# Kernel optimization log

Hardware: AMD Instinct MI355X
Metric: run time of the kernel (lower is better)

## Reference

```python
import jax, jax.numpy as jnp
import numpy as np

N_HEADS = 16
HEAD_DIM = 64
D_MODEL = N_HEADS * HEAD_DIM
MASK_NUM = -2.0**32 + 1.0
LN_EPS = 1e-8


def setup_inputs() -> dict:
    key = jax.random.key(0)
    ks = jax.random.split(key, 6)
    B, S = 2, 2048
    queries = jax.random.normal(ks[0], (B, S, D_MODEL), dtype=jnp.float32)
    keys = jax.random.normal(ks[1], (B, S, D_MODEL), dtype=jnp.float32)
    values = jax.random.normal(ks[2], (B, S, D_MODEL), dtype=jnp.float32)
    lim = np.sqrt(6.0 / (D_MODEL + D_MODEL)).astype(np.float32)  # glorot_uniform
    Wq = jax.random.uniform(ks[3], (D_MODEL, D_MODEL), jnp.float32, -lim, lim)
    Wk = jax.random.uniform(ks[4], (D_MODEL, D_MODEL), jnp.float32, -lim, lim)
    Wv = jax.random.uniform(ks[5], (D_MODEL, D_MODEL), jnp.float32, -lim, lim)
    gamma = jnp.ones((D_MODEL,), jnp.float32)
    beta = jnp.zeros((D_MODEL,), jnp.float32)
    return {"queries": queries, "keys": keys, "values": values,
            "Wq": Wq, "Wk": Wk, "Wv": Wv, "gamma": gamma, "beta": beta}


def _split_heads(x):
    # [B, S, H*dh] -> tf.split(axis=2)+concat(axis=0) order: [H*B, S, dh]
    B, S, _ = x.shape
    return x.reshape(B, S, N_HEADS, HEAD_DIM).transpose(2, 0, 1, 3).reshape(N_HEADS * B, S, HEAD_DIM)


def _merge_heads(x, B):
    # [H*B, S, dh] -> [B, S, H*dh]
    S = x.shape[1]
    return x.reshape(N_HEADS, B, S, HEAD_DIM).transpose(1, 2, 0, 3).reshape(B, S, D_MODEL)


def reference(queries, keys, values, Wq, Wk, Wv, gamma, beta):
    B = queries.shape[0]
    q = _split_heads(queries @ Wq)   # [HB, Sq, dh]
    k = _split_heads(keys @ Wk)      # [HB, Sk, dh]
    v = _split_heads(values @ Wv)    # [HB, Sk, dh]

    scores = jnp.einsum('bqd,bkd->bqk', q, k) / jnp.float32(np.sqrt(HEAD_DIM))
    # key padding mask: positions whose projected key is all-zero
    kmask = jnp.sign(jnp.sum(jnp.abs(k), axis=-1))  # [HB, Sk]
    scores = jnp.where(kmask[:, None, :] == 0, jnp.float32(MASK_NUM), scores)
    attn = jax.nn.softmax(scores, axis=-1)
    # query mask: zero out rows whose projected query is all-zero
    qmask = jnp.sign(jnp.sum(jnp.abs(q), axis=-1))  # [HB, Sq]
    attn = attn * qmask[:, :, None]
    att_out = jnp.einsum('bqk,bkd->bqd', attn, v)   # [HB, Sq, dh]
    att_out = _merge_heads(att_out, B)               # [B, Sq, D]

    x = att_out + queries
    mean = jnp.mean(x, axis=-1, keepdims=True)
    var = jnp.mean((x - mean) ** 2, axis=-1, keepdims=True)
    norm = (x - mean) / jnp.sqrt(var + LN_EPS)
    return gamma * norm + beta
```

## Files before the change

### kernel.cpp

```cpp
#include <hip/hip_runtime.h>

#define DM   1024
#define SEQ  2048
#define NH   16
#define HD   64
#define ROWS 4096

typedef unsigned short u16;
typedef unsigned int   u32;
typedef __attribute__((ext_vector_type(8))) __bf16 bf16x8;
typedef __attribute__((ext_vector_type(4))) float  f32x4;
typedef __attribute__((ext_vector_type(16))) float f32x16;

__device__ __forceinline__ u16 f2bf(float f) {
  u32 u = __builtin_bit_cast(u32, f);
  u += 0x7fffu + ((u >> 16) & 1u);
  return (u16)(u >> 16);
}

__device__ __forceinline__ void async16(const void* g, void* lds) {
  __builtin_amdgcn_global_load_lds((const __attribute__((address_space(1))) u32*)g,
                                   (__attribute__((address_space(3))) u32*)lds, 16, 0, 0);
}


__global__ __launch_bounds__(256) void k_cvt_act(const float* __restrict__ q,
                                                 const float* __restrict__ k,
                                                 const float* __restrict__ v,
                                                 u16* __restrict__ dst) {
  const float* src = blockIdx.z == 0 ? q : (blockIdx.z == 1 ? k : v);
  u16* d = dst + (size_t)blockIdx.z * ((size_t)ROWS * DM);
  size_t i = ((size_t)blockIdx.x * 256 + threadIdx.x) * 8;
  float4 a = *(const float4*)(src + i);
  float4 b = *(const float4*)(src + i + 4);
  u32 w0 = (u32)f2bf(a.x) | ((u32)f2bf(a.y) << 16);
  u32 w1 = (u32)f2bf(a.z) | ((u32)f2bf(a.w) << 16);
  u32 w2 = (u32)f2bf(b.x) | ((u32)f2bf(b.y) << 16);
  u32 w3 = (u32)f2bf(b.z) | ((u32)f2bf(b.w) << 16);
  uint4 o4; o4.x = w0; o4.y = w1; o4.z = w2; o4.w = w3;
  *(uint4*)(d + i) = o4;
}

__global__ __launch_bounds__(256) void k_cvt_wt(const float* __restrict__ Wq,
                                                const float* __restrict__ Wk,
                                                const float* __restrict__ Wv,
                                                u16* __restrict__ wt) {
  __shared__ float t[32][33];
  const float* W = blockIdx.z == 0 ? Wq : (blockIdx.z == 1 ? Wk : Wv);
  u16* D = wt + (size_t)blockIdx.z * (DM * DM);
  int bx = blockIdx.x * 32, by = blockIdx.y * 32;
  int x = threadIdx.x, y = threadIdx.y;
  for (int i = 0; i < 32; i += 8) t[y + i][x] = W[(size_t)(by + y + i) * DM + bx + x];
  __syncthreads();
  for (int i = 0; i < 32; i += 8) D[(size_t)(bx + y + i) * DM + by + x] = f2bf(t[x][y + i]);
}


__global__ __launch_bounds__(256) void k_gemm(const u16* __restrict__ Abase,
                                              const u16* __restrict__ Btbase,
                                              u16* __restrict__ Cbase) {
  __shared__ u16 As[128 * 32];
  __shared__ u16 Bs[128 * 32];
  const int z = blockIdx.z;
  const u16* A  = Abase  + (size_t)z * ((size_t)ROWS * DM);
  const u16* Bt = Btbase + (size_t)z * (DM * DM);
  u16* C        = Cbase  + (size_t)z * ((size_t)ROWS * DM);
  const float sc = (z == 0) ? 0.18033688011112043f : 1.0f;
  int tid = threadIdx.x, w = tid >> 6, l = tid & 63;
  int fr = l & 15, fq = l >> 4;
  int bid = blockIdx.y * 8 + blockIdx.x;
  int nb  = (bid & 7) * 32 + (bid >> 3);
  int m0 = (nb >> 3) * 128, n0 = (nb & 7) * 128;
  int wr = (w >> 1) * 64, wc = (w & 1) * 64;
  f32x4 acc[4][4];
  for (int i = 0; i < 4; ++i) for (int j = 0; j < 4; ++j) acc[i][j] = (f32x4){0.f, 0.f, 0.f, 0.f};

  for (int k0 = 0; k0 < DM; k0 += 32) {
    __syncthreads();
    for (int c = 0; c < 2; ++c) {
      int loff = (c * 4 + w) * 1024;
      int eoff = (loff >> 1) + l * 8;
      int row = eoff >> 5;
      int blk = (eoff & 31) >> 3;
      int gblk = blk ^ ((row >> 1) & 3);
      async16(A  + (size_t)(m0 + row) * DM + k0 + (gblk << 3), (char*)As + loff);
      async16(Bt + (size_t)(n0 + row) * DM + k0 + (gblk << 3), (char*)Bs + loff);
    }
    __syncthreads();
    bf16x8 af[4], bf[4];
    for (int i = 0; i < 4; ++i) {
      int row = wr + i * 16 + fr;
      af[i] = *(const bf16x8*)(As + row * 32 + ((fq ^ ((row >> 1) & 3)) << 3));
    }
    for (int j = 0; j < 4; ++j) {
      int row = wc + j * 16 + fr;
      bf[j] = *(const bf16x8*)(Bs + row * 32 + ((fq ^ ((row >> 1) & 3)) << 3));
    }
    for (int i = 0; i < 4; ++i)
      for (int j = 0; j < 4; ++j)
        acc[i][j] = __builtin_amdgcn_mfma_f32_16x16x32_bf16(af[i], bf[j], acc[i][j], 0, 0, 0);
  }
  for (int i = 0; i < 4; ++i)
    for (int j = 0; j < 4; ++j)
      for (int jj = 0; jj < 4; ++jj) {
        int row = m0 + wr + i * 16 + fq * 4 + jj;
        int col = n0 + wc + j * 16 + fr;
        C[(size_t)row * DM + col] = f2bf(acc[i][j][jj] * sc);
      }
}


__global__ __launch_bounds__(256) void k_vt(const u16* __restrict__ vproj,
                                            u16* __restrict__ vt) {
  __shared__ u16 t[64][64];
  int y = blockIdx.y;
  int h = y >> 1, b = y & 1;
  int s0 = blockIdx.x * 64;
  int tid = threadIdx.x;
  for (int c = 0; c < 2; ++c) {
    int rr = c * 32 + (tid >> 3);
    int blk = tid & 7;
    uint4 vv = *(const uint4*)(vproj + (size_t)(b * SEQ + s0 + rr) * DM + h * 64 + blk * 8);
    *(uint4*)(&t[rr][((blk ^ (rr & 7)) * 8)]) = vv;
  }
  __syncthreads();
  for (int c = 0; c < 2; ++c) {
    int d = c * 32 + (tid >> 3);
    int p = tid & 7;
    int B = p ^ (d & 7);
    int g = B >> 1, half = B & 1;
    u16 tmp[8];
    for (int j = 0; j < 8; ++j) {
      int kj = (j < 4) ? (4 * half + j) : (8 + 4 * half + (j - 4));
      int ss = 16 * g + kj;
      tmp[j] = t[ss][((d >> 3) ^ (ss & 7)) * 8 + (d & 7)];
    }
    *(uint4*)(vt + (size_t)(y * 64 + d) * SEQ + s0 + p * 8) = *(uint4*)tmp;
  }
}


__global__ __launch_bounds__(256, 2) void k_attn(const u16* __restrict__ Qp,
                                                 const u16* __restrict__ Kp,
                                                 const u16* __restrict__ Vt,
                                                 float* __restrict__ att) {
  __shared__ u16 lds[20480];
  const int tid = threadIdx.x, w = tid >> 6, l = tid & 63;
  const int lrow = l & 31, h = l >> 5;
  const int kh = w & 1, qg = w >> 1;
  const int g = blockIdx.x;
  const int vy = (g & 7) * 4 + ((g >> 3) & 3);
  const int vx = g >> 5;
  const int head = vy >> 1, b = vy & 1;
  const int hcol = head * 64;
  const int q0w = vx * 128 + qg * 64;

  bf16x8 qb00, qb01, qb02, qb03, qb10, qb11, qb12, qb13;
  {
    const u16* qr0 = Qp + (size_t)(b * SEQ + q0w + lrow) * DM + hcol + h * 8;
    qb00 = *(const bf16x8*)(qr0);
    qb01 = *(const bf16x8*)(qr0 + 16);
    qb02 = *(const bf16x8*)(qr0 + 32);
    qb03 = *(const bf16x8*)(qr0 + 48);
    const u16* qr1 = Qp + (size_t)(b * SEQ + q0w + 32 + lrow) * DM + hcol + h * 8;
    qb10 = *(const bf16x8*)(qr1);
    qb11 = *(const bf16x8*)(qr1 + 16);
    qb12 = *(const bf16x8*)(qr1 + 32);
    qb13 = *(const bf16x8*)(qr1 + 48);
  }

  const int sw = lrow & 7;
  const int kbase = kh * 4096 + lrow * 128;
  const int B0 = kbase + (((0 + h) ^ sw) << 4);
  const int B1 = kbase + (((2 + h) ^ sw) << 4);
  const int B2 = kbase + (((4 + h) ^ sw) << 4);
  const int B3 = kbase + (((6 + h) ^ sw) << 4);

  const int vfb = lrow * 128;
  const int V0 = vfb + (((4 * kh + 0 + h) ^ sw) << 4);
  const int V1 = vfb + (((4 * kh + 2 + h) ^ sw) << 4);

  const int ldo0 = w * 1024, ldo1 = (4 + w) * 1024;
  const int e0 = (ldo0 >> 1) + l * 8, e1 = (ldo1 >> 1) + l * 8;
  const int r0 = e0 >> 6, r1 = e1 >> 6;
  const int kb0 = ((e0 & 63) >> 3) ^ (r0 & 7), kb1 = ((e1 & 63) >> 3) ^ (r1 & 7);
  const u32 koff0 = (u32)((b * SEQ + r0) * DM + hcol + kb0 * 8);
  const u32 koff1 = (u32)((b * SEQ + r1) * DM + hcol + kb1 * 8);
  const u32 voff0 = (u32)((vy * 64 + r0) * SEQ + (e0 & 63));
  const u32 voff1 = (u32)((vy * 64 + r1) * SEQ + (e1 & 63));

  const f32x16 kzero = {};
  f32x16 ot00 = {}, ot01 = {}, ot10 = {}, ot11 = {};
  float lacc0 = 0.f, lacc1 = 0.f;
  bf16x8 pb00 = {}, pb01 = {}, pb10 = {}, pb11 = {};

  char* base = (char*)lds;
  async16(Kp + koff0, base + ldo0);
  async16(Kp + koff1, base + ldo1);
  async16(Vt + voff0, base + 16384 + ldo0);
  async16(Vt + voff1, base + 16384 + ldo1);

  int vwr = 1, vcr = 0, vrd = 2;
  for (int t = 0; t < SEQ / 64; ++t) {
    {
      u32 u = (t + 1 < SEQ / 64) ? (u32)(t + 1) : (u32)(SEQ / 64 - 1);
      u32 kadv = u * (64 * DM);
      u32 vadv = u * 64;
      char* kd = base + ((t + 1) & 1) * 8192;
      char* vd = base + 16384 + vwr * 8192;
      async16(Kp + kadv + koff0, kd + ldo0);
      async16(Kp + kadv + koff1, kd + ldo1);
      async16(Vt + vadv + voff0, vd + ldo0);
      async16(Vt + vadv + voff1, vd + ldo1);
    }
    asm volatile("s_waitcnt vmcnt(6)" ::: "memory");
    __builtin_amdgcn_s_barrier();
    asm volatile("" ::: "memory");

    const char* Kb = base + (t & 1) * 8192;
    bf16x8 a0 = *(const bf16x8*)(Kb + B0);
    bf16x8 a1 = *(const bf16x8*)(Kb + B1);
    bf16x8 a2 = *(const bf16x8*)(Kb + B2);
    bf16x8 a3 = *(const bf16x8*)(Kb + B3);
    __builtin_amdgcn_s_setprio(1);
    f32x16 st0 = __builtin_amdgcn_mfma_f32_32x32x16_bf16(a0, qb00, kzero, 0, 0, 0);
    f32x16 st1 = __builtin_amdgcn_mfma_f32_32x32x16_bf16(a0, qb10, kzero, 0, 0, 0);
    st0 = __builtin_amdgcn_mfma_f32_32x32x16_bf16(a1, qb01, st0, 0, 0, 0);
    st1 = __builtin_amdgcn_mfma_f32_32x32x16_bf16(a1, qb11, st1, 0, 0, 0);
    st0 = __builtin_amdgcn_mfma_f32_32x32x16_bf16(a2, qb02, st0, 0, 0, 0);
    st1 = __builtin_amdgcn_mfma_f32_32x32x16_bf16(a2, qb12, st1, 0, 0, 0);
    st0 = __builtin_amdgcn_mfma_f32_32x32x16_bf16(a3, qb03, st0, 0, 0, 0);
    st1 = __builtin_amdgcn_mfma_f32_32x32x16_bf16(a3, qb13, st1, 0, 0, 0);
    __builtin_amdgcn_s_setprio(0);

    if (t) {
      const char* Vb = base + 16384 + vrd * 8192;
      bf16x8 vf0 = *(const bf16x8*)(Vb + V0);
      bf16x8 vf1 = *(const bf16x8*)(Vb + V1);
      bf16x8 vf2 = *(const bf16x8*)(Vb + 4096 + V0);
      bf16x8 vf3 = *(const bf16x8*)(Vb + 4096 + V1);
      __builtin_amdgcn_s_setprio(1);
      ot00 = __builtin_amdgcn_mfma_f32_32x32x16_bf16(vf0, pb00, ot00, 0, 0, 0);
      ot10 = __builtin_amdgcn_mfma_f32_32x32x16_bf16(vf0, pb10, ot10, 0, 0, 0);
      ot00 = __builtin_amdgcn_mfma_f32_32x32x16_bf16(vf1, pb01, ot00, 0, 0, 0);
      ot10 = __builtin_amdgcn_mfma_f32_32x32x16_bf16(vf1, pb11, ot10, 0, 0, 0);
      ot01 = __builtin_amdgcn_mfma_f32_32x32x16_bf16(vf2, pb00, ot01, 0, 0, 0);
      ot11 = __builtin_amdgcn_mfma_f32_32x32x16_bf16(vf2, pb10, ot11, 0, 0, 0);
      ot01 = __builtin_amdgcn_mfma_f32_32x32x16_bf16(vf3, pb01, ot01, 0, 0, 0);
      ot11 = __builtin_amdgcn_mfma_f32_32x32x16_bf16(vf3, pb11, ot11, 0, 0, 0);
      __builtin_amdgcn_s_setprio(0);
    }

    {
      f32x16 p;
#pragma unroll
      for (int i = 0; i < 16; ++i) p[i] = __builtin_amdgcn_exp2f(st0[i]);
      float s0 = (p[0] + p[1]) + (p[2] + p[3]);
      float s1 = (p[4] + p[5]) + (p[6] + p[7]);
      float s2 = (p[8] + p[9]) + (p[10] + p[11]);
      float s3 = (p[12] + p[13]) + (p[14] + p[15]);
      lacc0 += (s0 + s1) + (s2 + s3);
#pragma unroll
      for (int j = 0; j < 8; ++j) { pb00[j] = (__bf16)p[j]; pb01[j] = (__bf16)p[8 + j]; }
    }
    {
      f32x16 p;
#pragma unroll
      for (int i = 0; i < 16; ++i) p[i] = __builtin_amdgcn_exp2f(st1[i]);
      float s0 = (p[0] + p[1]) + (p[2] + p[3]);
      float s1 = (p[4] + p[5]) + (p[6] + p[7]);
      float s2 = (p[8] + p[9]) + (p[10] + p[11]);
      float s3 = (p[12] + p[13]) + (p[14] + p[15]);
      lacc1 += (s0 + s1) + (s2 + s3);
#pragma unroll
      for (int j = 0; j < 8; ++j) { pb10[j] = (__bf16)p[j]; pb11[j] = (__bf16)p[8 + j]; }
    }

    asm volatile("" ::: "memory");
    __builtin_amdgcn_s_barrier();
    asm volatile("" ::: "memory");

    int tmp = vrd; vrd = vcr; vcr = vwr; vwr = tmp;
  }

  asm volatile("s_waitcnt vmcnt(0)" ::: "memory");
  __builtin_amdgcn_s_barrier();
  asm volatile("" ::: "memory");
  {
    const char* Vb = base + 16384 + vrd * 8192;
    bf16x8 vf0 = *(const bf16x8*)(Vb + V0);
    bf16x8 vf1 = *(const bf16x8*)(Vb + V1);
    bf16x8 vf2 = *(const bf16x8*)(Vb + 4096 + V0);
    bf16x8 vf3 = *(const bf16x8*)(Vb + 4096 + V1);
    ot00 = __builtin_amdgcn_mfma_f32_32x32x16_bf16(vf0, pb00, ot00, 0, 0, 0);
    ot10 = __builtin_amdgcn_mfma_f32_32x32x16_bf16(vf0, pb10, ot10, 0, 0, 0);
    ot00 = __builtin_amdgcn_mfma_f32_32x32x16_bf16(vf1, pb01, ot00, 0, 0, 0);
    ot10 = __builtin_amdgcn_mfma_f32_32x32x16_bf16(vf1, pb11, ot10, 0, 0, 0);
    ot01 = __builtin_amdgcn_mfma_f32_32x32x16_bf16(vf2, pb00, ot01, 0, 0, 0);
    ot11 = __builtin_amdgcn_mfma_f32_32x32x16_bf16(vf2, pb10, ot11, 0, 0, 0);
    ot01 = __builtin_amdgcn_mfma_f32_32x32x16_bf16(vf3, pb01, ot01, 0, 0, 0);
    ot11 = __builtin_amdgcn_mfma_f32_32x32x16_bf16(vf3, pb11, ot11, 0, 0, 0);
  }
  lacc0 += __shfl_xor(lacc0, 32);
  lacc1 += __shfl_xor(lacc1, 32);

  __syncthreads();
  float* mrg = (float*)lds;
  const int slot = qg * 4352;
  if (kh) {
#pragma unroll
    for (int r = 0; r < 16; ++r) {
      mrg[slot + r * 64 + l] = ot00[r];
      mrg[slot + (16 + r) * 64 + l] = ot01[r];
      mrg[slot + (32 + r) * 64 + l] = ot10[r];
      mrg[slot + (48 + r) * 64 + l] = ot11[r];
    }
    mrg[slot + 4096 + l] = lacc0;
    mrg[slot + 4160 + l] = lacc1;
  }
  __syncthreads();
  if (!kh) {
    float inv0 = 1.f / (lacc0 + mrg[slot + 4096 + l]);
    float inv1 = 1.f / (lacc1 + mrg[slot + 4160 + l]);
    float* orow0 = att + (size_t)(b * SEQ + q0w + lrow) * DM + hcol + 4 * h;
    float* orow1 = att + (size_t)(b * SEQ + q0w + 32 + lrow) * DM + hcol + 4 * h;
#pragma unroll
    for (int G = 0; G < 4; ++G) {
      float4 w0;
      w0.x = (ot00[4 * G + 0] + mrg[slot + (4 * G + 0) * 64 + l]) * inv0;
      w0.y = (ot00[4 * G + 1] + mrg[slot + (4 * G + 1) * 64 + l]) * inv0;
      w0.z = (ot00[4 * G + 2] + mrg[slot + (4 * G + 2) * 64 + l]) * inv0;
      w0.w = (ot00[4 * G + 3] + mrg[slot + (4 * G + 3) * 64 + l]) * inv0;
      *(float4*)(orow0 + 8 * G) = w0;
      float4 w1;
      w1.x = (ot01[4 * G + 0] + mrg[slot + (16 + 4 * G + 0) * 64 + l]) * inv0;
      w1.y = (ot01[4 * G + 1] + mrg[slot + (16 + 4 * G + 1) * 64 + l]) * inv0;
      w1.z = (ot01[4 * G + 2] + mrg[slot + (16 + 4 * G + 2) * 64 + l]) * inv0;
      w1.w = (ot01[4 * G + 3] + mrg[slot + (16 + 4 * G + 3) * 64 + l]) * inv0;
      *(float4*)(orow0 + 32 + 8 * G) = w1;
      float4 w2;
      w2.x = (ot10[4 * G + 0] + mrg[slot + (32 + 4 * G + 0) * 64 + l]) * inv1;
      w2.y = (ot10[4 * G + 1] + mrg[slot + (32 + 4 * G + 1) * 64 + l]) * inv1;
      w2.z = (ot10[4 * G + 2] + mrg[slot + (32 + 4 * G + 2) * 64 + l]) * inv1;
      w2.w = (ot10[4 * G + 3] + mrg[slot + (32 + 4 * G + 3) * 64 + l]) * inv1;
      *(float4*)(orow1 + 8 * G) = w2;
      float4 w3;
      w3.x = (ot11[4 * G + 0] + mrg[slot + (48 + 4 * G + 0) * 64 + l]) * inv1;
      w3.y = (ot11[4 * G + 1] + mrg[slot + (48 + 4 * G + 1) * 64 + l]) * inv1;
      w3.z = (ot11[4 * G + 2] + mrg[slot + (48 + 4 * G + 2) * 64 + l]) * inv1;
      w3.w = (ot11[4 * G + 3] + mrg[slot + (48 + 4 * G + 3) * 64 + l]) * inv1;
      *(float4*)(orow1 + 32 + 8 * G) = w3;
    }
  }
}


__global__ __launch_bounds__(256) void k_ln(const float* __restrict__ att,
                                            const float* __restrict__ qin,
                                            const float* __restrict__ gamma,
                                            const float* __restrict__ beta,
                                            float* __restrict__ out) {
  __shared__ float rsum[4], rsum2[4];
  int row = blockIdx.x, t = threadIdx.x;
  size_t off = (size_t)row * DM + t * 4;
  float4 a = *(const float4*)(att + off);
  float4 q = *(const float4*)(qin + off);
  float4 x; x.x = a.x + q.x; x.y = a.y + q.y; x.z = a.z + q.z; x.w = a.w + q.w;
  float s = x.x + x.y + x.z + x.w;
  float s2 = x.x * x.x + x.y * x.y + x.z * x.z + x.w * x.w;
  for (int o2 = 1; o2 < 64; o2 <<= 1) { s += __shfl_xor(s, o2); s2 += __shfl_xor(s2, o2); }
  int w = t >> 6, l = t & 63;
  if (l == 0) { rsum[w] = s; rsum2[w] = s2; }
  __syncthreads();
  s = rsum[0] + rsum[1] + rsum[2] + rsum[3];
  s2 = rsum2[0] + rsum2[1] + rsum2[2] + rsum2[3];
  float mean = s * (1.f / DM);
  float var = s2 * (1.f / DM) - mean * mean;
  float rstd = rsqrtf(var + 1e-8f);
  float4 g = *(const float4*)(gamma + t * 4);
  float4 be = *(const float4*)(beta + t * 4);
  float4 r;
  r.x = (x.x - mean) * rstd * g.x + be.x;
  r.y = (x.y - mean) * rstd * g.y + be.y;
  r.z = (x.z - mean) * rstd * g.z + be.z;
  r.w = (x.w - mean) * rstd * g.w + be.w;
  *(float4*)(out + off) = r;
}


extern "C" void kernel_launch(void* const* d_in, const int* in_sizes, int n_in,
                              void* d_out, int out_size, void* d_ws, size_t ws_size,
                              hipStream_t stream) {
  (void)in_sizes; (void)n_in; (void)out_size; (void)ws_size;
  const float* q     = (const float*)d_in[0];
  const float* k     = (const float*)d_in[1];
  const float* v     = (const float*)d_in[2];
  const float* Wq    = (const float*)d_in[3];
  const float* Wk    = (const float*)d_in[4];
  const float* Wv    = (const float*)d_in[5];
  const float* gamma = (const float*)d_in[6];
  const float* beta  = (const float*)d_in[7];
  float* out = (float*)d_out;
  char* ws = (char*)d_ws;

  const size_t ACT_B = 3ull * ROWS * DM * 2;
  const size_t WT_B  = 3ull * DM * DM * 2;

  u16* actb  = (u16*)ws;
  u16* wtb   = (u16*)(ws + ACT_B);
  u16* projb = (u16*)(ws + ACT_B + WT_B);
  u16* vt    = (u16*)ws;
  float* att = (float*)(ws + 8ull * 1024 * 1024);

  k_cvt_act<<<dim3(2048, 1, 3), 256, 0, stream>>>(q, k, v, actb);
  k_cvt_wt<<<dim3(32, 32, 3), dim3(32, 8), 0, stream>>>(Wq, Wk, Wv, wtb);
  k_gemm<<<dim3(8, 32, 3), 256, 0, stream>>>(actb, wtb, projb);
  k_vt<<<dim3(SEQ / 64, NH * 2), 256, 0, stream>>>(projb + 2ull * ROWS * DM, vt);
  k_attn<<<512, 256, 0, stream>>>(projb, projb + (size_t)ROWS * DM, vt, att);
  k_ln<<<ROWS, 256, 0, stream>>>(att, q, gamma, beta, out);
}
```

Measured before the change: 110.8 us.

## Fuse fp32-to-bf16 activation conversion into GEMM and store attention output as bf16

The separate activation conversion kernel is removed. The projection GEMM now loads fp32 activations into registers, converts them to bf16 and writes them to swizzled LDS, prefetching the next k-tile into registers while the current one is consumed. The attention kernel also writes its output as bf16 instead of fp32, and the layernorm kernel reads that back, which halves the intermediate traffic at the cost of a small precision loss. The A operand path trades async global-to-LDS loads for register staging, so the GEMM gains VGPR pressure and some conversion ALU work.

Result: faster. 105.7 us (-4.6%).

```diff
diff --git a/kernel.cpp b/kernel.cpp
--- a/kernel.cpp
+++ b/kernel.cpp
@@ -21,24 +21,6 @@
 __device__ __forceinline__ void async16(const void* g, void* lds) {
   __builtin_amdgcn_global_load_lds((const __attribute__((address_space(1))) u32*)g,
                                    (__attribute__((address_space(3))) u32*)lds, 16, 0, 0);
-}
-
-
-__global__ __launch_bounds__(256) void k_cvt_act(const float* __restrict__ q,
-                                                 const float* __restrict__ k,
-                                                 const float* __restrict__ v,
-                                                 u16* __restrict__ dst) {
-  const float* src = blockIdx.z == 0 ? q : (blockIdx.z == 1 ? k : v);
-  u16* d = dst + (size_t)blockIdx.z * ((size_t)ROWS * DM);
-  size_t i = ((size_t)blockIdx.x * 256 + threadIdx.x) * 8;
-  float4 a = *(const float4*)(src + i);
-  float4 b = *(const float4*)(src + i + 4);
-  u32 w0 = (u32)f2bf(a.x) | ((u32)f2bf(a.y) << 16);
-  u32 w1 = (u32)f2bf(a.z) | ((u32)f2bf(a.w) << 16);
-  u32 w2 = (u32)f2bf(b.x) | ((u32)f2bf(b.y) << 16);
-  u32 w3 = (u32)f2bf(b.z) | ((u32)f2bf(b.w) << 16);
-  uint4 o4; o4.x = w0; o4.y = w1; o4.z = w2; o4.w = w3;
-  *(uint4*)(d + i) = o4;
 }
 
 __global__ __launch_bounds__(256) void k_cvt_wt(const float* __restrict__ Wq,
@@ -56,13 +38,15 @@
 }
 
 
-__global__ __launch_bounds__(256) void k_gemm(const u16* __restrict__ Abase,
+__global__ __launch_bounds__(256) void k_gemm(const float* __restrict__ qf,
+                                              const float* __restrict__ kf,
+                                              const float* __restrict__ vf,
                                               const u16* __restrict__ Btbase,
                                               u16* __restrict__ Cbase) {
   __shared__ u16 As[128 * 32];
   __shared__ u16 Bs[128 * 32];
   const int z = blockIdx.z;
-  const u16* A  = Abase  + (size_t)z * ((size_t)ROWS * DM);
+  const float* A = z == 0 ? qf : (z == 1 ? kf : vf);
   const u16* Bt = Btbase + (size_t)z * (DM * DM);
   u16* C        = Cbase  + (size_t)z * ((size_t)ROWS * DM);
   const float sc = (z == 0) ? 0.18033688011112043f : 1.0f;
@@ -75,6 +59,19 @@
   f32x4 acc[4][4];
   for (int i = 0; i < 4; ++i) for (int j = 0; j < 4; ++j) acc[i][j] = (f32x4){0.f, 0.f, 0.f, 0.f};
 
+  const int row0 = tid >> 2, blk0 = tid & 3;
+  const int row1 = row0 + 64;
+  const size_t abase0 = (size_t)(m0 + row0) * DM + blk0 * 8;
+  const size_t abase1 = (size_t)(m0 + row1) * DM + blk0 * 8;
+  const int awr0 = row0 * 32 + ((blk0 ^ ((row0 >> 1) & 3)) << 3);
+  const int awr1 = row1 * 32 + ((blk0 ^ ((row1 >> 1) & 3)) << 3);
+
+  float4 p0lo, p0hi, p1lo, p1hi;
+  p0lo = *(const float4*)(A + abase0);
+  p0hi = *(const float4*)(A + abase0 + 4);
+  p1lo = *(const float4*)(A + abase1);
+  p1hi = *(const float4*)(A + abase1 + 4);
+
   for (int k0 = 0; k0 < DM; k0 += 32) {
     __syncthreads();
     for (int c = 0; c < 2; ++c) {
@@ -83,10 +80,30 @@
       int row = eoff >> 5;
       int blk = (eoff & 31) >> 3;
       int gblk = blk ^ ((row >> 1) & 3);
-      async16(A  + (size_t)(m0 + row) * DM + k0 + (gblk << 3), (char*)As + loff);
       async16(Bt + (size_t)(n0 + row) * DM + k0 + (gblk << 3), (char*)Bs + loff);
     }
+    {
+      uint4 o;
+      o.x = (u32)f2bf(p0lo.x) | ((u32)f2bf(p0lo.y) << 16);
+      o.y = (u32)f2bf(p0lo.z) | ((u32)f2bf(p0lo.w) << 16);
+      o.z = (u32)f2bf(p0hi.x) | ((u32)f2bf(p0hi.y) << 16);
+      o.w = (u32)f2bf(p0hi.z) | ((u32)f2bf(p0hi.w) << 16);
+      *(uint4*)(As + awr0) = o;
+      uint4 o1;
+      o1.x = (u32)f2bf(p1lo.x) | ((u32)f2bf(p1lo.y) << 16);
+      o1.y = (u32)f2bf(p1lo.z) | ((u32)f2bf(p1lo.w) << 16);
+      o1.z = (u32)f2bf(p1hi.x) | ((u32)f2bf(p1hi.y) << 16);
+      o1.w = (u32)f2bf(p1hi.z) | ((u32)f2bf(p1hi.w) << 16);
+      *(uint4*)(As + awr1) = o1;
+    }
+    if (k0 + 32 < DM) {
+      p0lo = *(const float4*)(A + abase0 + k0 + 32);
+      p0hi = *(const float4*)(A + abase0 + k0 + 36);
+      p1lo = *(const float4*)(A + abase1 + k0 + 32);
+      p1hi = *(const float4*)(A + abase1 + k0 + 36);
+    }
     __syncthreads();
+
     bf16x8 af[4], bf[4];
     for (int i = 0; i < 4; ++i) {
       int row = wr + i * 16 + fr;
@@ -143,7 +160,7 @@
 __global__ __launch_bounds__(256, 2) void k_attn(const u16* __restrict__ Qp,
                                                  const u16* __restrict__ Kp,
                                                  const u16* __restrict__ Vt,
-                                                 float* __restrict__ att) {
+                                                 u16* __restrict__ attb) {
   __shared__ u16 lds[20480];
   const int tid = threadIdx.x, w = tid >> 6, l = tid & 63;
   const int lrow = l & 31, h = l >> 5;
@@ -322,40 +339,40 @@
   if (!kh) {
     float inv0 = 1.f / (lacc0 + mrg[slot + 4096 + l]);
     float inv1 = 1.f / (lacc1 + mrg[slot + 4160 + l]);
-    float* orow0 = att + (size_t)(b * SEQ + q0w + lrow) * DM + hcol + 4 * h;
-    float* orow1 = att + (size_t)(b * SEQ + q0w + 32 + lrow) * DM + hcol + 4 * h;
+    u16* orow0 = attb + (size_t)(b * SEQ + q0w + lrow) * DM + hcol + 4 * h;
+    u16* orow1 = attb + (size_t)(b * SEQ + q0w + 32 + lrow) * DM + hcol + 4 * h;
 #pragma unroll
     for (int G = 0; G < 4; ++G) {
-      float4 w0;
-      w0.x = (ot00[4 * G + 0] + mrg[slot + (4 * G + 0) * 64 + l]) * inv0;
-      w0.y = (ot00[4 * G + 1] + mrg[slot + (4 * G + 1) * 64 + l]) * inv0;
-      w0.z = (ot00[4 * G + 2] + mrg[slot + (4 * G + 2) * 64 + l]) * inv0;
-      w0.w = (ot00[4 * G + 3] + mrg[slot + (4 * G + 3) * 64 + l]) * inv0;
-      *(float4*)(orow0 + 8 * G) = w0;
-      float4 w1;
-      w1.x = (ot01[4 * G + 0] + mrg[slot + (16 + 4 * G + 0) * 64 + l]) * inv0;
-      w1.y = (ot01[4 * G + 1] + mrg[slot + (16 + 4 * G + 1) * 64 + l]) * inv0;
-      w1.z = (ot01[4 * G + 2] + mrg[slot + (16 + 4 * G + 2) * 64 + l]) * inv0;
-      w1.w = (ot01[4 * G + 3] + mrg[slot + (16 + 4 * G + 3) * 64 + l]) * inv0;
-      *(float4*)(orow0 + 32 + 8 * G) = w1;
-      float4 w2;
-      w2.x = (ot10[4 * G + 0] + mrg[slot + (32 + 4 * G + 0) * 64 + l]) * inv1;
-      w2.y = (ot10[4 * G + 1] + mrg[slot + (32 + 4 * G + 1) * 64 + l]) * inv1;
-      w2.z = (ot10[4 * G + 2] + mrg[slot + (32 + 4 * G + 2) * 64 + l]) * inv1;
-      w2.w = (ot10[4 * G + 3] + mrg[slot + (32 + 4 * G + 3) * 64 + l]) * inv1;
-      *(float4*)(orow1 + 8 * G) = w2;
-      float4 w3;
-      w3.x = (ot11[4 * G + 0] + mrg[slot + (48 + 4 * G + 0) * 64 + l]) * inv1;
-      w3.y = (ot11[4 * G + 1] + mrg[slot + (48 + 4 * G + 1) * 64 + l]) * inv1;
-      w3.z = (ot11[4 * G + 2] + mrg[slot + (48 + 4 * G + 2) * 64 + l]) * inv1;
-      w3.w = (ot11[4 * G + 3] + mrg[slot + (48 + 4 * G + 3) * 64 + l]) * inv1;
-      *(float4*)(orow1 + 32 + 8 * G) = w3;
-    }
-  }
-}
-
-
-__global__ __launch_bounds__(256) void k_ln(const float* __restrict__ att,
+      uint2 o;
+      o.x = (u32)f2bf((ot00[4*G+0] + mrg[slot + (4*G+0)*64 + l]) * inv0)
+          | ((u32)f2bf((ot00[4*G+1] + mrg[slot + (4*G+1)*64 + l]) * inv0) << 16);
+      o.y = (u32)f2bf((ot00[4*G+2] + mrg[slot + (4*G+2)*64 + l]) * inv0)
+          | ((u32)f2bf((ot00[4*G+3] + mrg[slot + (4*G+3)*64 + l]) * inv0) << 16);
+      *(uint2*)(orow0 + 8 * G) = o;
+      uint2 o1;
+      o1.x = (u32)f2bf((ot01[4*G+0] + mrg[slot + (16+4*G+0)*64 + l]) * inv0)
+           | ((u32)f2bf((ot01[4*G+1] + mrg[slot + (16+4*G+1)*64 + l]) * inv0) << 16);
+      o1.y = (u32)f2bf((ot01[4*G+2] + mrg[slot + (16+4*G+2)*64 + l]) * inv0)
+           | ((u32)f2bf((ot01[4*G+3] + mrg[slot + (16+4*G+3)*64 + l]) * inv0) << 16);
+      *(uint2*)(orow0 + 32 + 8 * G) = o1;
+      uint2 o2;
+      o2.x = (u32)f2bf((ot10[4*G+0] + mrg[slot + (32+4*G+0)*64 + l]) * inv1)
+           | ((u32)f2bf((ot10[4*G+1] + mrg[slot + (32+4*G+1)*64 + l]) * inv1) << 16);
+      o2.y = (u32)f2bf((ot10[4*G+2] + mrg[slot + (32+4*G+2)*64 + l]) * inv1)
+           | ((u32)f2bf((ot10[4*G+3] + mrg[slot + (32+4*G+3)*64 + l]) * inv1) << 16);
+      *(uint2*)(orow1 + 8 * G) = o2;
+      uint2 o3;
+      o3.x = (u32)f2bf((ot11[4*G+0] + mrg[slot + (48+4*G+0)*64 + l]) * inv1)
+           | ((u32)f2bf((ot11[4*G+1] + mrg[slot + (48+4*G+1)*64 + l]) * inv1) << 16);
+      o3.y = (u32)f2bf((ot11[4*G+2] + mrg[slot + (48+4*G+2)*64 + l]) * inv1)
+           | ((u32)f2bf((ot11[4*G+3] + mrg[slot + (48+4*G+3)*64 + l]) * inv1) << 16);
+      *(uint2*)(orow1 + 32 + 8 * G) = o3;
+    }
+  }
+}
+
+
+__global__ __launch_bounds__(256) void k_ln(const u16* __restrict__ attb,
                                             const float* __restrict__ qin,
                                             const float* __restrict__ gamma,
                                             const float* __restrict__ beta,
@@ -363,7 +380,12 @@
   __shared__ float rsum[4], rsum2[4];
   int row = blockIdx.x, t = threadIdx.x;
   size_t off = (size_t)row * DM + t * 4;
-  float4 a = *(const float4*)(att + off);
+  uint2 av = *(const uint2*)(attb + off);
+  float4 a;
+  a.x = __builtin_bit_cast(float, av.x << 16);
+  a.y = __builtin_bit_cast(float, av.x & 0xffff0000u);
+  a.z = __builtin_bit_cast(float, av.y << 16);
+  a.w = __builtin_bit_cast(float, av.y & 0xffff0000u);
   float4 q = *(const float4*)(qin + off);
   float4 x; x.x = a.x + q.x; x.y = a.y + q.y; x.z = a.z + q.z; x.w = a.w + q.w;
   float s = x.x + x.y + x.z + x.w;
@@ -403,19 +425,18 @@
   float* out = (float*)d_out;
   char* ws = (char*)d_ws;
 
-  const size_t ACT_B = 3ull * ROWS * DM * 2;
-  const size_t WT_B  = 3ull * DM * DM * 2;
-
-  u16* actb  = (u16*)ws;
-  u16* wtb   = (u16*)(ws + ACT_B);
-  u16* projb = (u16*)(ws + ACT_B + WT_B);
-  u16* vt    = (u16*)ws;
-  float* att = (float*)(ws + 8ull * 1024 * 1024);
-
-  k_cvt_act<<<dim3(2048, 1, 3), 256, 0, stream>>>(q, k, v, actb);
+  const size_t WT_B   = 3ull * DM * DM * 2;
+  const size_t PROJ_B = 3ull * ROWS * DM * 2;
+  const size_t VT_B   = (size_t)NH * 2 * HD * SEQ * 2;
+
+  u16* wtb   = (u16*)ws;
+  u16* projb = (u16*)(ws + WT_B);
+  u16* vt    = (u16*)(ws + WT_B + PROJ_B);
+  u16* attb  = (u16*)(ws + WT_B + PROJ_B + VT_B);
+
   k_cvt_wt<<<dim3(32, 32, 3), dim3(32, 8), 0, stream>>>(Wq, Wk, Wv, wtb);
-  k_gemm<<<dim3(8, 32, 3), 256, 0, stream>>>(actb, wtb, projb);
+  k_gemm<<<dim3(8, 32, 3), 256, 0, stream>>>(q, k, v, wtb, projb);
   k_vt<<<dim3(SEQ / 64, NH * 2), 256, 0, stream>>>(projb + 2ull * ROWS * DM, vt);
-  k_attn<<<512, 256, 0, stream>>>(projb, projb + (size_t)ROWS * DM, vt, att);
-  k_ln<<<ROWS, 256, 0, stream>>>(att, q, gamma, beta, out);
-}
+  k_attn<<<512, 256, 0, stream>>>(projb, projb + (size_t)ROWS * DM, vt, attb);
+  k_ln<<<ROWS, 256, 0, stream>>>(attb, q, gamma, beta, out);
+}
```
